# Performance work log

Measured on AMD Instinct MI355X. Metric: run time of the kernel, lower is better.

Reference implementation:

```python
import jax, jax.numpy as jnp
import numpy as np

VOCAB = 100000
EMBED = 64
HIDDEN = 256
SEQ = 200
BATCH = 4096


def setup_inputs() -> dict:
    key = jax.random.key(0)
    ks = jax.random.split(key, 12)
    s = 0.02
    return {
        "user_hist": jax.random.randint(ks[0], (BATCH, SEQ), 0, VOCAB),
        "target_item": jax.random.randint(ks[1], (BATCH,), 0, VOCAB),
        "user_emb": jax.random.normal(ks[2], (VOCAB, EMBED), jnp.float32) * s,
        "item_emb": jax.random.normal(ks[3], (VOCAB, EMBED), jnp.float32) * s,
        "attn_w1": jax.random.normal(ks[4], (4 * EMBED, HIDDEN), jnp.float32) * s,
        "attn_b1": jnp.zeros((HIDDEN,), jnp.float32),
        "attn_w2": jax.random.normal(ks[5], (HIDDEN, 1), jnp.float32) * s,
        "attn_b2": jnp.zeros((1,), jnp.float32),
        "mlp_w1": jax.random.normal(ks[6], (2 * EMBED, HIDDEN), jnp.float32) * s,
        "mlp_b1": jnp.zeros((HIDDEN,), jnp.float32),
        "mlp_w2": jax.random.normal(ks[7], (HIDDEN, 1), jnp.float32) * s,
        "mlp_b2": jnp.zeros((1,), jnp.float32),
    }


def reference(user_hist, target_item, user_emb, item_emb,
              attn_w1, attn_b1, attn_w2, attn_b2,
              mlp_w1, mlp_b1, mlp_w2, mlp_b2):
    # [B, S, E] history embeddings, [B, 1, E] target embedding
    h = user_emb[user_hist]
    t = item_emb[target_item][:, None, :]
    tb = jnp.broadcast_to(t, h.shape)
    # attention MLP over [B, S, 4E]
    att_in = jnp.concatenate([h, tb, h - t, h * t], axis=-1)
    att_h = jax.nn.relu(att_in @ attn_w1 + attn_b1)
    att_logits = (att_h @ attn_w2 + attn_b2)[..., 0]            # [B, S]
    att_w = jax.nn.softmax(att_logits, axis=-1)[..., None]      # [B, S, 1]
    user_interest = jnp.sum(h * att_w, axis=1)                  # [B, E]
    # prediction head on [B, 2E]
    mlp_in = jnp.concatenate([user_interest, t[:, 0, :]], axis=-1)
    mlp_h = jax.nn.relu(mlp_in @ mlp_w1 + mlp_b1)
    out = jax.nn.sigmoid(mlp_h @ mlp_w2 + mlp_b2)               # [B, 1]
    return out
```

## Files before the change

kernel.cpp:

```cpp
#include <hip/hip_runtime.h>
#include <math.h>

#define EMBED   64
#define HIDDEN  256
#define SEQ     200
#define SEQP    208
#define MT      13
#define VOCAB   100000

typedef _Float16 f16x8  __attribute__((ext_vector_type(8)));
typedef float    f32x4  __attribute__((ext_vector_type(4)));
typedef float    f32x2  __attribute__((ext_vector_type(2)));


__global__ void din_setup(const float* __restrict__ attn_w1,
                          const float* __restrict__ mlp_w1,
                          const float* __restrict__ user_emb,
                          uint2* __restrict__ fragB8,
                          _Float16* __restrict__ fragW3,
                          _Float16* __restrict__ fragDt,
                          _Float16* __restrict__ fragB2,
                          unsigned char* __restrict__ emb8,
                          int do_emb) {
  const int gid = blockIdx.x * 256 + threadIdx.x;
  if (gid < 2048) {
    const int i = gid >> 7, rem = gid & 127, kc = rem >> 6, lane = rem & 63;
    const int n = i * 16 + (lane & 15);
    const int kb = kc * 32 + (lane >> 4) * 8;
    float v[8];
    #pragma unroll
    for (int j = 0; j < 8; ++j)
      v[j] = 16.0f * (attn_w1[(kb + j) * HIDDEN + n] + attn_w1[(128 + kb + j) * HIDDEN + n]);
    int lo = __builtin_amdgcn_cvt_pk_fp8_f32(v[0], v[1], 0, false);
    lo     = __builtin_amdgcn_cvt_pk_fp8_f32(v[2], v[3], lo, true);
    int hi = __builtin_amdgcn_cvt_pk_fp8_f32(v[4], v[5], 0, false);
    hi     = __builtin_amdgcn_cvt_pk_fp8_f32(v[6], v[7], hi, true);
    fragB8[gid] = uint2{(unsigned)lo, (unsigned)hi};
  } else if (gid < 4096) {
    const int g = gid - 2048;
    const int i = g >> 7, rem = g & 127, kc = rem >> 6, lane = rem & 63;
    const int n = i * 16 + (lane & 15);
    const int kb = kc * 32 + (lane >> 4) * 8;
    #pragma unroll
    for (int j = 0; j < 8; ++j)
      fragW3[g * 8 + j] = (_Float16)(16.0f * attn_w1[(192 + kb + j) * HIDDEN + n]);
  } else if (gid < 6144) {
    const int g = gid - 4096;
    const int i = g >> 7, rem = g & 127, kc = rem >> 6, lane = rem & 63;
    const int n = i * 16 + (lane & 15);
    const int kb = kc * 32 + (lane >> 4) * 8;
    #pragma unroll
    for (int j = 0; j < 8; ++j)
      fragDt[g * 8 + j] = (_Float16)(attn_w1[(64 + kb + j) * HIDDEN + n]
                                   - attn_w1[(128 + kb + j) * HIDDEN + n]);
  } else if (gid < 10240) {
    const int g = gid - 6144;
    const int nt = g >> 8, kc = (g >> 6) & 3, lane = g & 63;
    const int n = nt * 16 + (lane & 15);
    const int kb = kc * 32 + (lane >> 4) * 8;
    #pragma unroll
    for (int j = 0; j < 8; ++j)
      fragB2[g * 8 + j] = (_Float16)mlp_w1[(kb + j) * HIDDEN + n];
  } else if (do_emb) {
    const int g = gid - 10240;
    if (g < VOCAB * EMBED / 8) {
      const int base = g * 8;
      const float4 x = *reinterpret_cast<const float4*>(&user_emb[base]);
      const float4 y = *reinterpret_cast<const float4*>(&user_emb[base + 4]);
      int lo = __builtin_amdgcn_cvt_pk_fp8_f32(16.f * x.x, 16.f * x.y, 0, false);
      lo     = __builtin_amdgcn_cvt_pk_fp8_f32(16.f * x.z, 16.f * x.w, lo, true);
      int hi = __builtin_amdgcn_cvt_pk_fp8_f32(16.f * y.x, 16.f * y.y, 0, false);
      hi     = __builtin_amdgcn_cvt_pk_fp8_f32(16.f * y.z, 16.f * y.w, hi, true);
      *reinterpret_cast<uint2*>(&emb8[base]) = uint2{(unsigned)lo, (unsigned)hi};
    }
  }
}

__global__ __launch_bounds__(256, 6)
void din_fused_kernel(const int* __restrict__ user_hist,
                      const int* __restrict__ target_item,
                      const float* __restrict__ user_emb,
                      const float* __restrict__ item_emb,
                      const float* __restrict__ attn_b1,
                      const float* __restrict__ attn_w2,
                      const float* __restrict__ mlp_b1,
                      const float* __restrict__ mlp_w2,
                      const float* __restrict__ mlp_b2,
                      const uint2* __restrict__ fragB8,
                      const _Float16* __restrict__ fragW3,
                      const _Float16* __restrict__ fragDt,
                      const _Float16* __restrict__ fragB2,
                      const unsigned char* __restrict__ emb8,
                      float* __restrict__ out)
{
  __shared__ __align__(16) uint2 Hf8[MT * 2 * 64];
  __shared__ float lpf[4][SEQP];
  __shared__ int   histL[SEQP];
  __shared__ float weights[SEQP];
  __shared__ __align__(16) _Float16 t16[EMBED];
  __shared__ __align__(16) _Float16 mi16[EMBED];
  __shared__ float red[8];

  const int b    = blockIdx.x;
  const int tid  = threadIdx.x;
  const int lane = tid & 63;
  const int wave = tid >> 6;
  const int m    = lane & 15;
  const int quad = lane >> 4;

  if (tid < EMBED) t16[tid] = (_Float16)item_emb[target_item[b] * EMBED + tid];
  if (tid < SEQP) histL[tid] = (tid < SEQ) ? user_hist[b * SEQ + tid] : 0;
  __syncthreads();

  if (emb8) {
    for (int slot = tid; slot < MT * 2 * 64; slot += 256) {
      const int ln = slot & 63, kcomb = slot >> 6;
      const int st = kcomb >> 1, kc = kcomb & 1;
      const int s = st * 16 + (ln & 15);
      const int kb = kc * 32 + (ln >> 4) * 8;
      uint2 pv = uint2{0u, 0u};
      if (s < SEQ)
        pv = *reinterpret_cast<const uint2*>(&emb8[histL[s] * EMBED + kb]);
      Hf8[slot] = pv;
    }
  } else {
    for (int slot = tid; slot < MT * 2 * 64; slot += 256) {
      const int ln = slot & 63, kcomb = slot >> 6;
      const int st = kcomb >> 1, kc = kcomb & 1;
      const int s = st * 16 + (ln & 15);
      const int kb = kc * 32 + (ln >> 4) * 8;
      uint2 pv = uint2{0u, 0u};
      if (s < SEQ) {
        const float4* src = reinterpret_cast<const float4*>(&user_emb[histL[s] * EMBED + kb]);
        const float4 x = src[0], y = src[1];
        int lo = __builtin_amdgcn_cvt_pk_fp8_f32(16.f * x.x, 16.f * x.y, 0, false);
        lo     = __builtin_amdgcn_cvt_pk_fp8_f32(16.f * x.z, 16.f * x.w, lo, true);
        int hi = __builtin_amdgcn_cvt_pk_fp8_f32(16.f * y.x, 16.f * y.y, 0, false);
        hi     = __builtin_amdgcn_cvt_pk_fp8_f32(16.f * y.z, 16.f * y.w, hi, true);
        pv = uint2{(unsigned)lo, (unsigned)hi};
      }
      Hf8[slot] = pv;
    }
  }

  const f16x8 tv0 = *reinterpret_cast<const f16x8*>(&t16[quad * 8]);
  const f16x8 tv1 = *reinterpret_cast<const f16x8*>(&t16[32 + quad * 8]);

  #pragma unroll 1
  for (int p = 0; p < 2; ++p) {
    long long Aw[2][2];
    float cn[2][4], w2n[2][4];
    #pragma unroll
    for (int i = 0; i < 2; ++i) {
      const int tile = wave * 4 + p * 2 + i;
      #pragma unroll
      for (int c = 0; c < 2; ++c) {
        const uint2 w8 = fragB8[(tile * 2 + c) * 64 + lane];
        const f32x2 e0 = __builtin_amdgcn_cvt_pk_f32_fp8((int)w8.x, false);
        const f32x2 e1 = __builtin_amdgcn_cvt_pk_f32_fp8((int)w8.x, true);
        const f32x2 e2 = __builtin_amdgcn_cvt_pk_f32_fp8((int)w8.y, false);
        const f32x2 e3 = __builtin_amdgcn_cvt_pk_f32_fp8((int)w8.y, true);
        const f16x8 w3v = reinterpret_cast<const f16x8*>(fragW3)[(tile * 2 + c) * 64 + lane];
        const f16x8 pp = w3v * (c ? tv1 : tv0);
        int lo = __builtin_amdgcn_cvt_pk_fp8_f32(e0.x + (float)pp[0], e0.y + (float)pp[1], 0, false);
        lo     = __builtin_amdgcn_cvt_pk_fp8_f32(e1.x + (float)pp[2], e1.y + (float)pp[3], lo, true);
        int hi = __builtin_amdgcn_cvt_pk_fp8_f32(e2.x + (float)pp[4], e2.y + (float)pp[5], 0, false);
        hi     = __builtin_amdgcn_cvt_pk_fp8_f32(e3.x + (float)pp[6], e3.y + (float)pp[7], hi, true);
        Aw[i][c] = __builtin_bit_cast(long long, uint2{(unsigned)lo, (unsigned)hi});
      }
      const f16x8 d0 = reinterpret_cast<const f16x8*>(fragDt)[(tile * 2 + 0) * 64 + lane];
      const f16x8 d1 = reinterpret_cast<const f16x8*>(fragDt)[(tile * 2 + 1) * 64 + lane];
      f32x4 acc = {0.f, 0.f, 0.f, 0.f};
      acc = __builtin_amdgcn_mfma_f32_16x16x32_f16(d0, tv0, acc, 0, 0, 0);
      acc = __builtin_amdgcn_mfma_f32_16x16x32_f16(d1, tv1, acc, 0, 0, 0);
      const int nb = tile * 16 + quad * 4;
      const float4 b1v = *reinterpret_cast<const float4*>(&attn_b1[nb]);
      const float4 w2v = *reinterpret_cast<const float4*>(&attn_w2[nb]);
      cn[i][0] = 256.0f * (b1v.x + acc[0]);
      cn[i][1] = 256.0f * (b1v.y + acc[1]);
      cn[i][2] = 256.0f * (b1v.z + acc[2]);
      cn[i][3] = 256.0f * (b1v.w + acc[3]);
      w2n[i][0] = w2v.x * (1.0f / 256.0f);
      w2n[i][1] = w2v.y * (1.0f / 256.0f);
      w2n[i][2] = w2v.z * (1.0f / 256.0f);
      w2n[i][3] = w2v.w * (1.0f / 256.0f);
    }

    if (p == 0) __syncthreads();

    #pragma unroll 2
    for (int st = 0; st < MT; ++st) {
      const long long b0 = __builtin_bit_cast(long long, Hf8[(st * 2 + 0) * 64 + lane]);
      const long long b1 = __builtin_bit_cast(long long, Hf8[(st * 2 + 1) * 64 + lane]);
      float lg = 0.f;
      #pragma unroll
      for (int i = 0; i < 2; ++i) {
        f32x4 acc = {cn[i][0], cn[i][1], cn[i][2], cn[i][3]};
        acc = __builtin_amdgcn_mfma_f32_16x16x32_fp8_fp8(Aw[i][0], b0, acc, 0, 0, 0);
        acc = __builtin_amdgcn_mfma_f32_16x16x32_fp8_fp8(Aw[i][1], b1, acc, 0, 0, 0);
        #pragma unroll
        for (int q = 0; q < 4; ++q)
          lg += fmaxf(acc[q], 0.0f) * w2n[i][q];
      }
      lg += __shfl_xor(lg, 16, 64);
      lg += __shfl_xor(lg, 32, 64);
      if (lane < 16) {
        if (p == 0) lpf[wave][st * 16 + lane] = lg;
        else        lpf[wave][st * 16 + lane] += lg;
      }
    }
  }
  __syncthreads();

  float v = -INFINITY, e = 0.0f;
  if (tid < SEQ)
    v = lpf[0][tid] + lpf[1][tid] + lpf[2][tid] + lpf[3][tid];
  {
    float mx = v;
    #pragma unroll
    for (int off = 32; off; off >>= 1) mx = fmaxf(mx, __shfl_xor(mx, off, 64));
    if (lane == 0) red[wave] = mx;
  }
  __syncthreads();
  {
    const float mx = fmaxf(fmaxf(red[0], red[1]), fmaxf(red[2], red[3]));
    e = (tid < SEQ) ? expf(v - mx) : 0.0f;
    float ssum = e;
    #pragma unroll
    for (int off = 32; off; off >>= 1) ssum += __shfl_xor(ssum, off, 64);
    if (lane == 0) red[4 + wave] = ssum;
  }
  __syncthreads();
  {
    const float tot = red[4] + red[5] + red[6] + red[7];
    if (tid < SEQP) weights[tid] = (tid < SEQ) ? e / tot : 0.0f;
  }
  __syncthreads();

  {
    const int kc = wave & 1, g2 = wave >> 1;
    float pk[8];
    #pragma unroll
    for (int j = 0; j < 8; ++j) pk[j] = 0.f;
    #pragma unroll
    for (int st2 = 0; st2 < 7; ++st2) {
      const int st = g2 + 2 * st2;
      if (st < MT) {
        const float wt = weights[st * 16 + m];
        const uint2 hv = Hf8[(st * 2 + kc) * 64 + lane];
        const f32x2 f0 = __builtin_amdgcn_cvt_pk_f32_fp8((int)hv.x, false);
        const f32x2 f1 = __builtin_amdgcn_cvt_pk_f32_fp8((int)hv.x, true);
        const f32x2 f2 = __builtin_amdgcn_cvt_pk_f32_fp8((int)hv.y, false);
        const f32x2 f3 = __builtin_amdgcn_cvt_pk_f32_fp8((int)hv.y, true);
        pk[0] += wt * f0.x;  pk[1] += wt * f0.y;
        pk[2] += wt * f1.x;  pk[3] += wt * f1.y;
        pk[4] += wt * f2.x;  pk[5] += wt * f2.y;
        pk[6] += wt * f3.x;  pk[7] += wt * f3.y;
      }
    }
    #pragma unroll
    for (int j = 0; j < 8; ++j) {
      float p = pk[j];
      p += __shfl_xor(p, 1, 64);
      p += __shfl_xor(p, 2, 64);
      p += __shfl_xor(p, 4, 64);
      p += __shfl_xor(p, 8, 64);
      pk[j] = p;
    }
    if (m == 0) {
      float* ip = &lpf[0][0];
      #pragma unroll
      for (int j = 0; j < 8; ++j)
        ip[g2 * 64 + kc * 32 + quad * 8 + j] = pk[j];
    }
  }
  __syncthreads();
  if (tid < EMBED) {
    const float* ip = &lpf[0][0];
    mi16[tid] = (_Float16)((ip[tid] + ip[64 + tid]) * 0.0625f);
  }
  __syncthreads();

  {
    const f16x8 mb0 = *reinterpret_cast<const f16x8*>(&mi16[quad * 8]);
    const f16x8 mb1 = *reinterpret_cast<const f16x8*>(&mi16[32 + quad * 8]);
    float z = 0.f;
    #pragma unroll
    for (int i = 0; i < 4; ++i) {
      const int tt = wave * 4 + i;
      const f16x8* B2 = reinterpret_cast<const f16x8*>(fragB2) + (tt * 4) * 64 + lane;
      const int nb = tt * 16 + quad * 4;
      const float4 bb = *reinterpret_cast<const float4*>(&mlp_b1[nb]);
      const float4 ww = *reinterpret_cast<const float4*>(&mlp_w2[nb]);
      f32x4 acc = {bb.x, bb.y, bb.z, bb.w};
      acc = __builtin_amdgcn_mfma_f32_16x16x32_f16(B2[0],   mb0, acc, 0, 0, 0);
      acc = __builtin_amdgcn_mfma_f32_16x16x32_f16(B2[64],  mb1, acc, 0, 0, 0);
      acc = __builtin_amdgcn_mfma_f32_16x16x32_f16(B2[128], tv0, acc, 0, 0, 0);
      acc = __builtin_amdgcn_mfma_f32_16x16x32_f16(B2[192], tv1, acc, 0, 0, 0);
      z += fmaxf(acc[0], 0.0f) * ww.x;
      z += fmaxf(acc[1], 0.0f) * ww.y;
      z += fmaxf(acc[2], 0.0f) * ww.z;
      z += fmaxf(acc[3], 0.0f) * ww.w;
    }
    z += __shfl_xor(z, 16, 64);
    z += __shfl_xor(z, 32, 64);
    if (lane == 0) red[wave] = z;
  }
  __syncthreads();
  if (tid == 0) {
    const float zz = red[0] + red[1] + red[2] + red[3] + mlp_b2[0];
    out[b] = 1.0f / (1.0f + expf(-zz));
  }
}

extern "C" void kernel_launch(void* const* d_in, const int* in_sizes, int n_in,
                              void* d_out, int out_size, void* d_ws, size_t ws_size,
                              hipStream_t stream) {
  const int*   user_hist   = (const int*)  d_in[0];
  const int*   target_item = (const int*)  d_in[1];
  const float* user_emb    = (const float*)d_in[2];
  const float* item_emb    = (const float*)d_in[3];
  const float* attn_w1     = (const float*)d_in[4];
  const float* attn_b1     = (const float*)d_in[5];
  const float* attn_w2     = (const float*)d_in[6];
  const float* mlp_w1      = (const float*)d_in[8];
  const float* mlp_b1      = (const float*)d_in[9];
  const float* mlp_w2      = (const float*)d_in[10];
  const float* mlp_b2      = (const float*)d_in[11];
  float* out = (float*)d_out;

  uint2*    fragB8 = (uint2*)d_ws;
  _Float16* fragW3 = (_Float16*)((char*)d_ws + 16384);
  _Float16* fragDt = (_Float16*)((char*)d_ws + 49152);
  _Float16* fragB2 = (_Float16*)((char*)d_ws + 81920);
  const size_t emb8_off = 147456;
  const size_t emb8_bytes = (size_t)VOCAB * EMBED;
  unsigned char* emb8 = nullptr;
  if (ws_size >= emb8_off + emb8_bytes)
    emb8 = (unsigned char*)d_ws + emb8_off;

  const int setup_gids = 10240 + VOCAB * EMBED / 8;
  din_setup<<<(setup_gids + 255) / 256, 256, 0, stream>>>(
      attn_w1, mlp_w1, user_emb, fragB8, fragW3, fragDt, fragB2,
      emb8 ? emb8 : (unsigned char*)d_ws, emb8 ? 1 : 0);

  const int batch = in_sizes[1];
  din_fused_kernel<<<batch, 256, 0, stream>>>(
      user_hist, target_item, user_emb, item_emb,
      attn_b1, attn_w2, mlp_b1, mlp_w2, mlp_b2,
      fragB8, fragW3, fragDt, fragB2, emb8, out);
}
```

Baseline: 169.0 us.

## Compute all four hidden tiles per wave in one pass with fp16 weight folding

```diff
diff --git a/kernel.cpp b/kernel.cpp
--- a/kernel.cpp
+++ b/kernel.cpp
@@ -9,6 +9,7 @@
 #define VOCAB   100000
 
 typedef _Float16 f16x8  __attribute__((ext_vector_type(8)));
+typedef _Float16 f16x2  __attribute__((ext_vector_type(2)));
 typedef float    f32x4  __attribute__((ext_vector_type(4)));
 typedef float    f32x2  __attribute__((ext_vector_type(2)));
 
@@ -16,7 +17,7 @@
 __global__ void din_setup(const float* __restrict__ attn_w1,
                           const float* __restrict__ mlp_w1,
                           const float* __restrict__ user_emb,
-                          uint2* __restrict__ fragB8,
+                          _Float16* __restrict__ fragW16,
                           _Float16* __restrict__ fragW3,
                           _Float16* __restrict__ fragDt,
                           _Float16* __restrict__ fragB2,
@@ -27,15 +28,10 @@
     const int i = gid >> 7, rem = gid & 127, kc = rem >> 6, lane = rem & 63;
     const int n = i * 16 + (lane & 15);
     const int kb = kc * 32 + (lane >> 4) * 8;
-    float v[8];
     #pragma unroll
     for (int j = 0; j < 8; ++j)
-      v[j] = 16.0f * (attn_w1[(kb + j) * HIDDEN + n] + attn_w1[(128 + kb + j) * HIDDEN + n]);
-    int lo = __builtin_amdgcn_cvt_pk_fp8_f32(v[0], v[1], 0, false);
-    lo     = __builtin_amdgcn_cvt_pk_fp8_f32(v[2], v[3], lo, true);
-    int hi = __builtin_amdgcn_cvt_pk_fp8_f32(v[4], v[5], 0, false);
-    hi     = __builtin_amdgcn_cvt_pk_fp8_f32(v[6], v[7], hi, true);
-    fragB8[gid] = uint2{(unsigned)lo, (unsigned)hi};
+      fragW16[gid * 8 + j] = (_Float16)(16.0f * (attn_w1[(kb + j) * HIDDEN + n]
+                                               + attn_w1[(128 + kb + j) * HIDDEN + n]));
   } else if (gid < 4096) {
     const int g = gid - 2048;
     const int i = g >> 7, rem = g & 127, kc = rem >> 6, lane = rem & 63;
@@ -86,7 +82,7 @@
                       const float* __restrict__ mlp_b1,
                       const float* __restrict__ mlp_w2,
                       const float* __restrict__ mlp_b2,
-                      const uint2* __restrict__ fragB8,
+                      const _Float16* __restrict__ fragW16,
                       const _Float16* __restrict__ fragW3,
                       const _Float16* __restrict__ fragDt,
                       const _Float16* __restrict__ fragB2,
@@ -94,7 +90,7 @@
                       float* __restrict__ out)
 {
   __shared__ __align__(16) uint2 Hf8[MT * 2 * 64];
-  __shared__ float lpf[4][SEQP];
+  __shared__ __align__(16) _Float16 lpq[SEQP][16];
   __shared__ int   histL[SEQP];
   __shared__ float weights[SEQP];
   __shared__ __align__(16) _Float16 t16[EMBED];
@@ -112,109 +108,103 @@
   if (tid < SEQP) histL[tid] = (tid < SEQ) ? user_hist[b * SEQ + tid] : 0;
   __syncthreads();
 
+  const int s0  = (wave >> 1) * 16 + m;
+  const int kb0 = (wave & 1) * 32 + quad * 8;
   if (emb8) {
-    for (int slot = tid; slot < MT * 2 * 64; slot += 256) {
-      const int ln = slot & 63, kcomb = slot >> 6;
-      const int st = kcomb >> 1, kc = kcomb & 1;
-      const int s = st * 16 + (ln & 15);
-      const int kb = kc * 32 + (ln >> 4) * 8;
-      uint2 pv = uint2{0u, 0u};
-      if (s < SEQ)
-        pv = *reinterpret_cast<const uint2*>(&emb8[histL[s] * EMBED + kb]);
-      Hf8[slot] = pv;
+    #pragma unroll
+    for (int i = 0; i < 7; ++i) {
+      const int s = s0 + 32 * i;
+      if (s < SEQP) {
+        uint2 pv = uint2{0u, 0u};
+        if (s < SEQ)
+          pv = *reinterpret_cast<const uint2*>(&emb8[histL[s] * EMBED + kb0]);
+        Hf8[tid + 256 * i] = pv;
+      }
     }
   } else {
-    for (int slot = tid; slot < MT * 2 * 64; slot += 256) {
-      const int ln = slot & 63, kcomb = slot >> 6;
-      const int st = kcomb >> 1, kc = kcomb & 1;
-      const int s = st * 16 + (ln & 15);
-      const int kb = kc * 32 + (ln >> 4) * 8;
-      uint2 pv = uint2{0u, 0u};
-      if (s < SEQ) {
-        const float4* src = reinterpret_cast<const float4*>(&user_emb[histL[s] * EMBED + kb]);
-        const float4 x = src[0], y = src[1];
-        int lo = __builtin_amdgcn_cvt_pk_fp8_f32(16.f * x.x, 16.f * x.y, 0, false);
-        lo     = __builtin_amdgcn_cvt_pk_fp8_f32(16.f * x.z, 16.f * x.w, lo, true);
-        int hi = __builtin_amdgcn_cvt_pk_fp8_f32(16.f * y.x, 16.f * y.y, 0, false);
-        hi     = __builtin_amdgcn_cvt_pk_fp8_f32(16.f * y.z, 16.f * y.w, hi, true);
-        pv = uint2{(unsigned)lo, (unsigned)hi};
+    #pragma unroll
+    for (int i = 0; i < 7; ++i) {
+      const int s = s0 + 32 * i;
+      if (s < SEQP) {
+        uint2 pv = uint2{0u, 0u};
+        if (s < SEQ) {
+          const float4* src = reinterpret_cast<const float4*>(&user_emb[histL[s] * EMBED + kb0]);
+          const float4 x = src[0], y = src[1];
+          int lo = __builtin_amdgcn_cvt_pk_fp8_f32(16.f * x.x, 16.f * x.y, 0, false);
+          lo     = __builtin_amdgcn_cvt_pk_fp8_f32(16.f * x.z, 16.f * x.w, lo, true);
+          int hi = __builtin_amdgcn_cvt_pk_fp8_f32(16.f * y.x, 16.f * y.y, 0, false);
+          hi     = __builtin_amdgcn_cvt_pk_fp8_f32(16.f * y.z, 16.f * y.w, hi, true);
+          pv = uint2{(unsigned)lo, (unsigned)hi};
+        }
+        Hf8[tid + 256 * i] = pv;
       }
-      Hf8[slot] = pv;
-    }
-  }
-
-  const f16x8 tv0 = *reinterpret_cast<const f16x8*>(&t16[quad * 8]);
-  const f16x8 tv1 = *reinterpret_cast<const f16x8*>(&t16[32 + quad * 8]);
-
-  #pragma unroll 1
-  for (int p = 0; p < 2; ++p) {
-    long long Aw[2][2];
-    float cn[2][4], w2n[2][4];
-    #pragma unroll
-    for (int i = 0; i < 2; ++i) {
-      const int tile = wave * 4 + p * 2 + i;
+    }
+  }
+
+  long long Aw[4][2];
+  f32x4 cn4[4];
+  float w2n[4][4];
+  {
+    const f16x8 tv0 = *reinterpret_cast<const f16x8*>(&t16[quad * 8]);
+    const f16x8 tv1 = *reinterpret_cast<const f16x8*>(&t16[32 + quad * 8]);
+    #pragma unroll
+    for (int i = 0; i < 4; ++i) {
+      const int tile = wave * 4 + i;
       #pragma unroll
       for (int c = 0; c < 2; ++c) {
-        const uint2 w8 = fragB8[(tile * 2 + c) * 64 + lane];
-        const f32x2 e0 = __builtin_amdgcn_cvt_pk_f32_fp8((int)w8.x, false);
-        const f32x2 e1 = __builtin_amdgcn_cvt_pk_f32_fp8((int)w8.x, true);
-        const f32x2 e2 = __builtin_amdgcn_cvt_pk_f32_fp8((int)w8.y, false);
-        const f32x2 e3 = __builtin_amdgcn_cvt_pk_f32_fp8((int)w8.y, true);
+        const f16x8 w16 = reinterpret_cast<const f16x8*>(fragW16)[(tile * 2 + c) * 64 + lane];
         const f16x8 w3v = reinterpret_cast<const f16x8*>(fragW3)[(tile * 2 + c) * 64 + lane];
-        const f16x8 pp = w3v * (c ? tv1 : tv0);
-        int lo = __builtin_amdgcn_cvt_pk_fp8_f32(e0.x + (float)pp[0], e0.y + (float)pp[1], 0, false);
-        lo     = __builtin_amdgcn_cvt_pk_fp8_f32(e1.x + (float)pp[2], e1.y + (float)pp[3], lo, true);
-        int hi = __builtin_amdgcn_cvt_pk_fp8_f32(e2.x + (float)pp[4], e2.y + (float)pp[5], 0, false);
-        hi     = __builtin_amdgcn_cvt_pk_fp8_f32(e3.x + (float)pp[6], e3.y + (float)pp[7], hi, true);
+        const f16x8 p = w3v * (c ? tv1 : tv0) + w16;
+        int lo = __builtin_amdgcn_cvt_pk_fp8_f32((float)p[0], (float)p[1], 0, false);
+        lo     = __builtin_amdgcn_cvt_pk_fp8_f32((float)p[2], (float)p[3], lo, true);
+        int hi = __builtin_amdgcn_cvt_pk_fp8_f32((float)p[4], (float)p[5], 0, false);
+        hi     = __builtin_amdgcn_cvt_pk_fp8_f32((float)p[6], (float)p[7], hi, true);
         Aw[i][c] = __builtin_bit_cast(long long, uint2{(unsigned)lo, (unsigned)hi});
       }
       const f16x8 d0 = reinterpret_cast<const f16x8*>(fragDt)[(tile * 2 + 0) * 64 + lane];
       const f16x8 d1 = reinterpret_cast<const f16x8*>(fragDt)[(tile * 2 + 1) * 64 + lane];
-      f32x4 acc = {0.f, 0.f, 0.f, 0.f};
-      acc = __builtin_amdgcn_mfma_f32_16x16x32_f16(d0, tv0, acc, 0, 0, 0);
+      const f32x4 z = {0.f, 0.f, 0.f, 0.f};
+      f32x4 acc = __builtin_amdgcn_mfma_f32_16x16x32_f16(d0, tv0, z, 0, 0, 0);
       acc = __builtin_amdgcn_mfma_f32_16x16x32_f16(d1, tv1, acc, 0, 0, 0);
       const int nb = tile * 16 + quad * 4;
       const float4 b1v = *reinterpret_cast<const float4*>(&attn_b1[nb]);
       const float4 w2v = *reinterpret_cast<const float4*>(&attn_w2[nb]);
-      cn[i][0] = 256.0f * (b1v.x + acc[0]);
-      cn[i][1] = 256.0f * (b1v.y + acc[1]);
-      cn[i][2] = 256.0f * (b1v.z + acc[2]);
-      cn[i][3] = 256.0f * (b1v.w + acc[3]);
+      cn4[i][0] = 256.0f * (b1v.x + acc[0]);
+      cn4[i][1] = 256.0f * (b1v.y + acc[1]);
+      cn4[i][2] = 256.0f * (b1v.z + acc[2]);
+      cn4[i][3] = 256.0f * (b1v.w + acc[3]);
       w2n[i][0] = w2v.x * (1.0f / 256.0f);
       w2n[i][1] = w2v.y * (1.0f / 256.0f);
       w2n[i][2] = w2v.z * (1.0f / 256.0f);
       w2n[i][3] = w2v.w * (1.0f / 256.0f);
     }
-
-    if (p == 0) __syncthreads();
-
-    #pragma unroll 2
-    for (int st = 0; st < MT; ++st) {
-      const long long b0 = __builtin_bit_cast(long long, Hf8[(st * 2 + 0) * 64 + lane]);
-      const long long b1 = __builtin_bit_cast(long long, Hf8[(st * 2 + 1) * 64 + lane]);
-      float lg = 0.f;
-      #pragma unroll
-      for (int i = 0; i < 2; ++i) {
-        f32x4 acc = {cn[i][0], cn[i][1], cn[i][2], cn[i][3]};
-        acc = __builtin_amdgcn_mfma_f32_16x16x32_fp8_fp8(Aw[i][0], b0, acc, 0, 0, 0);
-        acc = __builtin_amdgcn_mfma_f32_16x16x32_fp8_fp8(Aw[i][1], b1, acc, 0, 0, 0);
-        #pragma unroll
-        for (int q = 0; q < 4; ++q)
-          lg += fmaxf(acc[q], 0.0f) * w2n[i][q];
-      }
-      lg += __shfl_xor(lg, 16, 64);
-      lg += __shfl_xor(lg, 32, 64);
-      if (lane < 16) {
-        if (p == 0) lpf[wave][st * 16 + lane] = lg;
-        else        lpf[wave][st * 16 + lane] += lg;
-      }
-    }
+  }
+  __syncthreads();
+
+  #pragma unroll 1
+  for (int st = 0; st < MT; ++st) {
+    const long long b0 = __builtin_bit_cast(long long, Hf8[(st * 2 + 0) * 64 + lane]);
+    const long long b1 = __builtin_bit_cast(long long, Hf8[(st * 2 + 1) * 64 + lane]);
+    float lg = 0.f;
+    #pragma unroll
+    for (int i = 0; i < 4; ++i) {
+      f32x4 acc = __builtin_amdgcn_mfma_f32_16x16x32_fp8_fp8(Aw[i][0], b0, cn4[i], 0, 0, 0);
+      acc = __builtin_amdgcn_mfma_f32_16x16x32_fp8_fp8(Aw[i][1], b1, acc, 0, 0, 0);
+      lg += fmaxf(acc[0], 0.0f) * w2n[i][0] + fmaxf(acc[1], 0.0f) * w2n[i][1]
+          + fmaxf(acc[2], 0.0f) * w2n[i][2] + fmaxf(acc[3], 0.0f) * w2n[i][3];
+    }
+    lpq[st * 16 + m][wave * 4 + quad] = (_Float16)lg;
   }
   __syncthreads();
 
   float v = -INFINITY, e = 0.0f;
-  if (tid < SEQ)
-    v = lpf[0][tid] + lpf[1][tid] + lpf[2][tid] + lpf[3][tid];
+  if (tid < SEQ) {
+    const f16x8 ra = *reinterpret_cast<const f16x8*>(&lpq[tid][0]);
+    const f16x8 rb = *reinterpret_cast<const f16x8*>(&lpq[tid][8]);
+    const f16x8 s8 = ra + rb;
+    v = (float)s8[0] + (float)s8[1] + (float)s8[2] + (float)s8[3]
+      + (float)s8[4] + (float)s8[5] + (float)s8[6] + (float)s8[7];
+  }
   {
     float mx = v;
     #pragma unroll
@@ -258,32 +248,35 @@
         pk[6] += wt * f3.x;  pk[7] += wt * f3.y;
       }
     }
-    #pragma unroll
-    for (int j = 0; j < 8; ++j) {
-      float p = pk[j];
-      p += __shfl_xor(p, 1, 64);
-      p += __shfl_xor(p, 2, 64);
-      p += __shfl_xor(p, 4, 64);
-      p += __shfl_xor(p, 8, 64);
-      pk[j] = p;
+    f16x2 hh[4];
+    #pragma unroll
+    for (int k = 0; k < 4; ++k)
+      hh[k] = __builtin_bit_cast(f16x2, __builtin_amdgcn_cvt_pkrtz(pk[2 * k], pk[2 * k + 1]));
+    #pragma unroll
+    for (int off = 1; off <= 8; off <<= 1) {
+      #pragma unroll
+      for (int k = 0; k < 4; ++k)
+        hh[k] += __builtin_bit_cast(f16x2, __shfl_xor(__builtin_bit_cast(int, hh[k]), off, 64));
     }
     if (m == 0) {
-      float* ip = &lpf[0][0];
+      _Float16* ip16 = &lpq[0][0];
       #pragma unroll
-      for (int j = 0; j < 8; ++j)
-        ip[g2 * 64 + kc * 32 + quad * 8 + j] = pk[j];
+      for (int k = 0; k < 4; ++k)
+        *reinterpret_cast<f16x2*>(&ip16[g2 * 64 + kc * 32 + quad * 8 + 2 * k]) = hh[k];
     }
   }
   __syncthreads();
   if (tid < EMBED) {
-    const float* ip = &lpf[0][0];
-    mi16[tid] = (_Float16)((ip[tid] + ip[64 + tid]) * 0.0625f);
+    const _Float16* ip16 = &lpq[0][0];
+    mi16[tid] = (_Float16)(((float)ip16[tid] + (float)ip16[64 + tid]) * 0.0625f);
   }
   __syncthreads();
 
   {
     const f16x8 mb0 = *reinterpret_cast<const f16x8*>(&mi16[quad * 8]);
     const f16x8 mb1 = *reinterpret_cast<const f16x8*>(&mi16[32 + quad * 8]);
+    const f16x8 tw0 = *reinterpret_cast<const f16x8*>(&t16[quad * 8]);
+    const f16x8 tw1 = *reinterpret_cast<const f16x8*>(&t16[32 + quad * 8]);
     float z = 0.f;
     #pragma unroll
     for (int i = 0; i < 4; ++i) {
@@ -295,8 +288,8 @@
       f32x4 acc = {bb.x, bb.y, bb.z, bb.w};
       acc = __builtin_amdgcn_mfma_f32_16x16x32_f16(B2[0],   mb0, acc, 0, 0, 0);
       acc = __builtin_amdgcn_mfma_f32_16x16x32_f16(B2[64],  mb1, acc, 0, 0, 0);
-      acc = __builtin_amdgcn_mfma_f32_16x16x32_f16(B2[128], tv0, acc, 0, 0, 0);
-      acc = __builtin_amdgcn_mfma_f32_16x16x32_f16(B2[192], tv1, acc, 0, 0, 0);
+      acc = __builtin_amdgcn_mfma_f32_16x16x32_f16(B2[128], tw0, acc, 0, 0, 0);
+      acc = __builtin_amdgcn_mfma_f32_16x16x32_f16(B2[192], tw1, acc, 0, 0, 0);
       z += fmaxf(acc[0], 0.0f) * ww.x;
       z += fmaxf(acc[1], 0.0f) * ww.y;
       z += fmaxf(acc[2], 0.0f) * ww.z;
@@ -329,11 +322,11 @@
   const float* mlp_b2      = (const float*)d_in[11];
   float* out = (float*)d_out;
 
-  uint2*    fragB8 = (uint2*)d_ws;
-  _Float16* fragW3 = (_Float16*)((char*)d_ws + 16384);
-  _Float16* fragDt = (_Float16*)((char*)d_ws + 49152);
-  _Float16* fragB2 = (_Float16*)((char*)d_ws + 81920);
-  const size_t emb8_off = 147456;
+  _Float16* fragW16 = (_Float16*)d_ws;
+  _Float16* fragW3  = (_Float16*)((char*)d_ws + 32768);
+  _Float16* fragDt  = (_Float16*)((char*)d_ws + 65536);
+  _Float16* fragB2  = (_Float16*)((char*)d_ws + 98304);
+  const size_t emb8_off = 163840;
   const size_t emb8_bytes = (size_t)VOCAB * EMBED;
   unsigned char* emb8 = nullptr;
   if (ws_size >= emb8_off + emb8_bytes)
@@ -341,12 +334,12 @@
 
   const int setup_gids = 10240 + VOCAB * EMBED / 8;
   din_setup<<<(setup_gids + 255) / 256, 256, 0, stream>>>(
-      attn_w1, mlp_w1, user_emb, fragB8, fragW3, fragDt, fragB2,
+      attn_w1, mlp_w1, user_emb, fragW16, fragW3, fragDt, fragB2,
       emb8 ? emb8 : (unsigned char*)d_ws, emb8 ? 1 : 0);
 
   const int batch = in_sizes[1];
   din_fused_kernel<<<batch, 256, 0, stream>>>(
       user_hist, target_item, user_emb, item_emb,
       attn_b1, attn_w2, mlp_b1, mlp_w2, mlp_b2,
-      fragB8, fragW3, fragDt, fragB2, emb8, out);
+      fragW16, fragW3, fragDt, fragB2, emb8, out);
 }
```

Measured after the change: 170.7 us. No clear change (+1.0%).
